# Performance work log

Hardware: AMD Instinct MI355X
Metric: run time of the kernel (lower is better)

## Reference

```python
import jax, jax.numpy as jnp
import numpy as np

B, C, H, W_, N, E = 8, 256, 128, 128, 4096, 128
EPS = 1e-12  # torch F.normalize default eps


def grid_sample_points(x, kpts):
    """Bilinear grid_sample at point coords, padding_mode='zeros', align_corners=False.
    x: [B,C,H,W], kpts: [B,N,2] in [-1,1] (x,y order) -> [B,C,N].
    """
    Bx, Cx, Hx, Wx = x.shape
    # unnormalize (align_corners=False)
    ix = (kpts[..., 0] + 1.0) * (Wx * 0.5) - 0.5  # [B,N]
    iy = (kpts[..., 1] + 1.0) * (Hx * 0.5) - 0.5
    x0f = jnp.floor(ix)
    y0f = jnp.floor(iy)
    wx = ix - x0f  # fractional weights
    wy = iy - y0f
    x0 = x0f.astype(jnp.int32)
    y0 = y0f.astype(jnp.int32)
    x1 = x0 + 1
    y1 = y0 + 1

    def gather(xi, yi):
        valid = (xi >= 0) & (xi < Wx) & (yi >= 0) & (yi < Hx)  # [B,N]
        xc = jnp.clip(xi, 0, Wx - 1)
        yc = jnp.clip(yi, 0, Hx - 1)
        # per-batch gather of [C] vectors at N points -> [B,C,N]
        v = jax.vmap(lambda xb, yy, xx: xb[:, yy, xx])(x, yc, xc)
        return v * valid[:, None, :].astype(x.dtype)

    v00 = gather(x0, y0)
    v10 = gather(x1, y0)
    v01 = gather(x0, y1)
    v11 = gather(x1, y1)
    wxb = wx[:, None, :]
    wyb = wy[:, None, :]
    return (v00 * (1 - wxb) * (1 - wyb)
            + v10 * wxb * (1 - wyb)
            + v01 * (1 - wxb) * wyb
            + v11 * wxb * wyb)


def setup_inputs() -> dict:
    key = jax.random.key(0)
    k1, k2, k3 = jax.random.split(key, 3)
    x = jax.random.normal(k1, (B, C, H, W_), dtype=jnp.float32)
    # keypoints in normalized [-1,1] coords (grid_sample convention)
    kpts = jax.random.uniform(k2, (B, N, 2), dtype=jnp.float32) * 2.0 - 1.0
    # xavier_normal_(gain=0.1) for Linear(C -> E)
    std = 0.1 * np.sqrt(2.0 / (C + E))
    whiten_w = jax.random.normal(k3, (E, C), dtype=jnp.float32) * std
    whiten_b = jnp.zeros((E,), dtype=jnp.float32)
    return {"x": x, "kpts": kpts, "whiten_w": whiten_w, "whiten_b": whiten_b}


def reference(x, kpts, whiten_w, whiten_b):
    desc = grid_sample_points(x, kpts)              # [B,C,N]
    desc = jnp.transpose(desc, (0, 2, 1))           # [B,N,C]
    desc = jnp.einsum('bnc,ec->bne', desc, whiten_w) + whiten_b  # [B,N,E]
    norm = jnp.maximum(jnp.linalg.norm(desc, axis=2, keepdims=True), EPS)
    return desc / norm
```

## Files before the change

kernel.cpp:

```cpp
#include <hip/hip_runtime.h>
#include <hip/hip_bf16.h>
#include <math.h>

#define BB 8
#define CC 256
#define HH 128
#define WW 128
#define NN 4096
#define EE 128

#define WT_OFF   0
#define BASE_OFF 131072
#define WGT_OFF  262144
#define DESC_OFF 786432
#define WS_NEED  (786432ull + (unsigned long long)BB*CC*NN*4ull)

__global__ void coef_kernel(const float* __restrict__ kpts,
                            int* __restrict__ baseb, float4* __restrict__ wgt) {
  int i = blockIdx.x * blockDim.x + threadIdx.x;
  float kx = kpts[2 * i], ky = kpts[2 * i + 1];
  float ix = (kx + 1.f) * (WW * 0.5f) - 0.5f;
  float iy = (ky + 1.f) * (HH * 0.5f) - 0.5f;
  float x0f = floorf(ix), y0f = floorf(iy);
  float wx = ix - x0f, wy = iy - y0f;
  int x0 = (int)x0f, y0 = (int)y0f;
  float ax0 = (x0 >= 0 && x0 < WW) ? (1.f - wx) : 0.f;
  float ax1 = (x0 + 1 >= 0 && x0 + 1 < WW) ? wx : 0.f;
  float ay0 = (y0 >= 0 && y0 < HH) ? (1.f - wy) : 0.f;
  float ay1 = (y0 + 1 >= 0 && y0 + 1 < HH) ? wy : 0.f;
  int bx = min(max(x0, 0), WW - 2);
  int by = min(max(y0, 0), HH - 2);
  float a0 = 0.f, a1 = 0.f, c0 = 0.f, c1 = 0.f;
  if (x0 == bx) a0 += ax0; else if (x0 == bx + 1) a1 += ax0;
  if (x0 + 1 == bx) a0 += ax1; else if (x0 + 1 == bx + 1) a1 += ax1;
  if (y0 == by) c0 += ay0; else if (y0 == by + 1) c1 += ay0;
  if (y0 + 1 == by) c0 += ay1; else if (y0 + 1 == by + 1) c1 += ay1;
  baseb[i] = by * WW + bx;
  wgt[i] = make_float4(a0 * c0, a1 * c0, a0 * c1, a1 * c1);
}

__global__ void wtrans_kernel(const float* __restrict__ W, float* __restrict__ Wt) {
  int i = blockIdx.x * blockDim.x + threadIdx.x;
  int c = i >> 7, e = i & (EE - 1);
  Wt[i] = W[e * CC + c];
}

__global__ __launch_bounds__(256) void gather_kernel(
    const float* __restrict__ x, const int* __restrict__ baseb,
    const float4* __restrict__ wgt, float* __restrict__ desc) {
  __shared__ float plane[HH * WW];
  int blk = blockIdx.x;
  int b = blk >> 8;
  const float4* s4 = (const float4*)(x + ((size_t)blk << 14));
  float4* p4 = (float4*)plane;
  for (int i = threadIdx.x; i < (HH * WW / 4); i += 256) p4[i] = s4[i];
  __syncthreads();
  const int* bb = baseb + b * NN;
  const float4* wb = wgt + b * NN;
  float* dst = desc + ((size_t)blk << 12);
  for (int n = threadIdx.x; n < NN; n += 256) {
    int base = bb[n];
    float4 w = wb[n];
    float v = plane[base] * w.x + plane[base + 1] * w.y
            + plane[base + WW] * w.z + plane[base + WW + 1] * w.w;
    dst[n] = v;
  }
}

__global__ __launch_bounds__(256) void gemm_norm_kernel(
    const float* __restrict__ desc, const float* __restrict__ Wt,
    const float* __restrict__ bias, float* __restrict__ out) {
  __shared__ float4 A4s[32 * 32];
  __shared__ float4 W4s[32 * 32];
  int t = threadIdx.x;
  int blk = blockIdx.x;
  int b = blk >> 5;
  int n0 = (blk & 31) << 7;
  int te = t & 15, tn = t >> 4;
  float acc[8][8];
#pragma unroll
  for (int j = 0; j < 8; ++j)
#pragma unroll
    for (int k = 0; k < 8; ++k) acc[j][k] = 0.f;
  const float4* wt4 = (const float4*)Wt;
  const float4* d4 = (const float4*)desc;
  for (int cb = 0; cb < CC; cb += 32) {
    __syncthreads();
    int base4 = (b * CC + cb) * (NN / 4) + (n0 >> 2);
#pragma unroll
    for (int p = 0; p < 4; ++p) {
      int q = t + 256 * p;
      int cc = q >> 5, ii = q & 31;
      A4s[q] = d4[base4 + cc * (NN / 4) + ii];
      W4s[q] = wt4[(cb + cc) * (EE / 4) + ii];
    }
    __syncthreads();
    for (int cc = 0; cc < 32; ++cc) {
      float4 a0 = A4s[cc * 32 + tn * 2];
      float4 a1 = A4s[cc * 32 + tn * 2 + 1];
      float4 w0 = W4s[cc * 32 + te * 2];
      float4 w1 = W4s[cc * 32 + te * 2 + 1];
      float av[8] = {a0.x, a0.y, a0.z, a0.w, a1.x, a1.y, a1.z, a1.w};
      float wv[8] = {w0.x, w0.y, w0.z, w0.w, w1.x, w1.y, w1.z, w1.w};
#pragma unroll
      for (int j = 0; j < 8; ++j)
#pragma unroll
        for (int k = 0; k < 8; ++k) acc[j][k] += wv[j] * av[k];
    }
  }
  float4 bi0 = *(const float4*)&bias[te * 8];
  float4 bi1 = *(const float4*)&bias[te * 8 + 4];
  float bv[8] = {bi0.x, bi0.y, bi0.z, bi0.w, bi1.x, bi1.y, bi1.z, bi1.w};
#pragma unroll
  for (int j = 0; j < 8; ++j)
#pragma unroll
    for (int k = 0; k < 8; ++k) acc[j][k] += bv[j];
  float4* out4 = (float4*)out;
#pragma unroll
  for (int k = 0; k < 8; ++k) {
    float s = 0.f;
#pragma unroll
    for (int j = 0; j < 8; ++j) s += acc[j][k] * acc[j][k];
    s += __shfl_xor(s, 1); s += __shfl_xor(s, 2);
    s += __shfl_xor(s, 4); s += __shfl_xor(s, 8);
    float inv = 1.f / fmaxf(sqrtf(s), 1e-12f);
    int n = n0 + tn * 8 + k;
    size_t o = ((size_t)(b * NN + n) << 5) + te * 2;
    out4[o]     = make_float4(acc[0][k] * inv, acc[1][k] * inv, acc[2][k] * inv, acc[3][k] * inv);
    out4[o + 1] = make_float4(acc[4][k] * inv, acc[5][k] * inv, acc[6][k] * inv, acc[7][k] * inv);
  }
}

__global__ __launch_bounds__(128) void fused_fallback(
    const float* __restrict__ x, const float* __restrict__ kpts,
    const float* __restrict__ W, const float* __restrict__ bias,
    float* __restrict__ out) {
  __shared__ float dsc[CC];
  __shared__ float sred[2];
  int blk = blockIdx.x;
  int b = blk >> 12;
  float kx = kpts[2 * blk], ky = kpts[2 * blk + 1];
  float ix = (kx + 1.f) * (WW * 0.5f) - 0.5f;
  float iy = (ky + 1.f) * (HH * 0.5f) - 0.5f;
  float x0f = floorf(ix), y0f = floorf(iy);
  float wx = ix - x0f, wy = iy - y0f;
  int x0 = (int)x0f, y0 = (int)y0f;
  float ax0 = (x0 >= 0 && x0 < WW) ? (1.f - wx) : 0.f;
  float ax1 = (x0 + 1 >= 0 && x0 + 1 < WW) ? wx : 0.f;
  float ay0 = (y0 >= 0 && y0 < HH) ? (1.f - wy) : 0.f;
  float ay1 = (y0 + 1 >= 0 && y0 + 1 < HH) ? wy : 0.f;
  int bx = min(max(x0, 0), WW - 2);
  int by = min(max(y0, 0), HH - 2);
  float a0 = 0.f, a1 = 0.f, r0 = 0.f, r1 = 0.f;
  if (x0 == bx) a0 += ax0; else if (x0 == bx + 1) a1 += ax0;
  if (x0 + 1 == bx) a0 += ax1; else if (x0 + 1 == bx + 1) a1 += ax1;
  if (y0 == by) r0 += ay0; else if (y0 == by + 1) r1 += ay0;
  if (y0 + 1 == by) r0 += ay1; else if (y0 + 1 == by + 1) r1 += ay1;
  int base = by * WW + bx;
  float w00 = a0 * r0, w10 = a1 * r0, w01 = a0 * r1, w11 = a1 * r1;
  int t = threadIdx.x;
  const float* src = x + ((size_t)b << 22);
  for (int c = t; c < CC; c += 128) {
    const float* p = src + ((size_t)c << 14);
    dsc[c] = p[base] * w00 + p[base + 1] * w10 + p[base + WW] * w01 + p[base + WW + 1] * w11;
  }
  __syncthreads();
  float acc = bias[t];
  const float* wr = W + t * CC;
  for (int c = 0; c < CC; ++c) acc += wr[c] * dsc[c];
  float s = acc * acc;
  for (int m = 1; m < 64; m <<= 1) s += __shfl_xor(s, m);
  if ((t & 63) == 0) sred[t >> 6] = s;
  __syncthreads();
  float tot = sred[0] + sred[1];
  float inv = 1.f / fmaxf(sqrtf(tot), 1e-12f);
  out[((size_t)blk << 7) + t] = acc * inv;
}

extern "C" void kernel_launch(void* const* d_in, const int* in_sizes, int n_in,
                              void* d_out, int out_size, void* d_ws, size_t ws_size,
                              hipStream_t stream) {
  const float* x    = (const float*)d_in[0];
  const float* kpts = (const float*)d_in[1];
  const float* W    = (const float*)d_in[2];
  const float* bias = (const float*)d_in[3];
  float* out = (float*)d_out;
  if (ws_size >= WS_NEED) {
    char* ws = (char*)d_ws;
    float* Wt    = (float*)(ws + WT_OFF);
    int* baseb   = (int*)(ws + BASE_OFF);
    float4* wgt  = (float4*)(ws + WGT_OFF);
    float* desc  = (float*)(ws + DESC_OFF);
    coef_kernel<<<BB * NN / 128, 128, 0, stream>>>(kpts, baseb, wgt);
    wtrans_kernel<<<CC * EE / 256, 256, 0, stream>>>(W, Wt);
    gather_kernel<<<BB * CC, 256, 0, stream>>>(x, baseb, wgt, desc);
    gemm_norm_kernel<<<BB * (NN / 128), 256, 0, stream>>>(desc, Wt, bias, out);
  } else {
    fused_fallback<<<BB * NN, 128, 0, stream>>>(x, kpts, W, bias, out);
  }
}
```

Baseline: 261.7 us.

## Merge prep kernels, widen gather blocks, shrink GEMM tiles for more blocks

Merges the coefficient and weight-transpose kernels into one prep kernel, which removes a launch. Doubles the gather kernel's block size to 512 threads and fully unrolls its loops. Retiles the GEMM+normalize kernel from 128-point tiles with 8x8 per-thread outputs to 64-point tiles with 4x4 per-thread outputs and 512 threads. This gives 512 blocks instead of 256 and lower register pressure, but less data reuse per thread.

```diff
diff --git a/kernel.cpp b/kernel.cpp
--- a/kernel.cpp
+++ b/kernel.cpp
@@ -15,9 +15,12 @@
 #define DESC_OFF 786432
 #define WS_NEED  (786432ull + (unsigned long long)BB*CC*NN*4ull)
 
-__global__ void coef_kernel(const float* __restrict__ kpts,
-                            int* __restrict__ baseb, float4* __restrict__ wgt) {
+__global__ __launch_bounds__(256) void prep_kernel(
+    const float* __restrict__ kpts, const float* __restrict__ W,
+    int* __restrict__ baseb, float4* __restrict__ wgt, float* __restrict__ Wt) {
   int i = blockIdx.x * blockDim.x + threadIdx.x;
+  int c = i >> 7, e = i & (EE - 1);
+  Wt[i] = W[e * CC + c];
   float kx = kpts[2 * i], ky = kpts[2 * i + 1];
   float ix = (kx + 1.f) * (WW * 0.5f) - 0.5f;
   float iy = (ky + 1.f) * (HH * 0.5f) - 0.5f;
@@ -39,95 +42,93 @@
   wgt[i] = make_float4(a0 * c0, a1 * c0, a0 * c1, a1 * c1);
 }
 
-__global__ void wtrans_kernel(const float* __restrict__ W, float* __restrict__ Wt) {
-  int i = blockIdx.x * blockDim.x + threadIdx.x;
-  int c = i >> 7, e = i & (EE - 1);
-  Wt[i] = W[e * CC + c];
-}
-
-__global__ __launch_bounds__(256) void gather_kernel(
+__global__ __launch_bounds__(512) void gather_kernel(
     const float* __restrict__ x, const int* __restrict__ baseb,
     const float4* __restrict__ wgt, float* __restrict__ desc) {
   __shared__ float plane[HH * WW];
   int blk = blockIdx.x;
   int b = blk >> 8;
+  int t = threadIdx.x;
   const float4* s4 = (const float4*)(x + ((size_t)blk << 14));
   float4* p4 = (float4*)plane;
-  for (int i = threadIdx.x; i < (HH * WW / 4); i += 256) p4[i] = s4[i];
+#pragma unroll
+  for (int i = 0; i < 8; ++i) p4[t + 512 * i] = s4[t + 512 * i];
   __syncthreads();
   const int* bb = baseb + b * NN;
   const float4* wb = wgt + b * NN;
   float* dst = desc + ((size_t)blk << 12);
-  for (int n = threadIdx.x; n < NN; n += 256) {
+#pragma unroll
+  for (int i = 0; i < 8; ++i) {
+    int n = t + 512 * i;
     int base = bb[n];
     float4 w = wb[n];
-    float v = plane[base] * w.x + plane[base + 1] * w.y
-            + plane[base + WW] * w.z + plane[base + WW + 1] * w.w;
-    dst[n] = v;
-  }
-}
-
-__global__ __launch_bounds__(256) void gemm_norm_kernel(
+    dst[n] = plane[base] * w.x + plane[base + 1] * w.y
+           + plane[base + WW] * w.z + plane[base + WW + 1] * w.w;
+  }
+}
+
+__global__ __launch_bounds__(512) void gemm_norm_kernel(
     const float* __restrict__ desc, const float* __restrict__ Wt,
     const float* __restrict__ bias, float* __restrict__ out) {
-  __shared__ float4 A4s[32 * 32];
+  __shared__ float4 A4s[32 * 16];
   __shared__ float4 W4s[32 * 32];
   int t = threadIdx.x;
   int blk = blockIdx.x;
-  int b = blk >> 5;
-  int n0 = (blk & 31) << 7;
-  int te = t & 15, tn = t >> 4;
-  float acc[8][8];
-#pragma unroll
-  for (int j = 0; j < 8; ++j)
-#pragma unroll
-    for (int k = 0; k < 8; ++k) acc[j][k] = 0.f;
+  int b = blk >> 6;
+  int n0 = (blk & 63) << 6;
+  int te = t & 31;
+  int tn = t >> 5;
+  float acc[4][4];
+#pragma unroll
+  for (int j = 0; j < 4; ++j)
+#pragma unroll
+    for (int k = 0; k < 4; ++k) acc[j][k] = 0.f;
   const float4* wt4 = (const float4*)Wt;
   const float4* d4 = (const float4*)desc;
   for (int cb = 0; cb < CC; cb += 32) {
     __syncthreads();
     int base4 = (b * CC + cb) * (NN / 4) + (n0 >> 2);
-#pragma unroll
-    for (int p = 0; p < 4; ++p) {
-      int q = t + 256 * p;
+    {
+      int ccA = t >> 4, iiA = t & 15;
+      A4s[t] = d4[base4 + ccA * (NN / 4) + iiA];
+    }
+#pragma unroll
+    for (int p = 0; p < 2; ++p) {
+      int q = t + 512 * p;
       int cc = q >> 5, ii = q & 31;
-      A4s[q] = d4[base4 + cc * (NN / 4) + ii];
       W4s[q] = wt4[(cb + cc) * (EE / 4) + ii];
     }
     __syncthreads();
+#pragma unroll
     for (int cc = 0; cc < 32; ++cc) {
-      float4 a0 = A4s[cc * 32 + tn * 2];
-      float4 a1 = A4s[cc * 32 + tn * 2 + 1];
-      float4 w0 = W4s[cc * 32 + te * 2];
-      float4 w1 = W4s[cc * 32 + te * 2 + 1];
-      float av[8] = {a0.x, a0.y, a0.z, a0.w, a1.x, a1.y, a1.z, a1.w};
-      float wv[8] = {w0.x, w0.y, w0.z, w0.w, w1.x, w1.y, w1.z, w1.w};
-#pragma unroll
-      for (int j = 0; j < 8; ++j)
-#pragma unroll
-        for (int k = 0; k < 8; ++k) acc[j][k] += wv[j] * av[k];
+      float4 a = A4s[cc * 16 + tn];
+      float4 w = W4s[cc * 32 + te];
+      float av[4] = {a.x, a.y, a.z, a.w};
+      float wv[4] = {w.x, w.y, w.z, w.w};
+#pragma unroll
+      for (int j = 0; j < 4; ++j)
+#pragma unroll
+        for (int k = 0; k < 4; ++k) acc[j][k] += wv[j] * av[k];
     }
   }
-  float4 bi0 = *(const float4*)&bias[te * 8];
-  float4 bi1 = *(const float4*)&bias[te * 8 + 4];
-  float bv[8] = {bi0.x, bi0.y, bi0.z, bi0.w, bi1.x, bi1.y, bi1.z, bi1.w};
-#pragma unroll
-  for (int j = 0; j < 8; ++j)
-#pragma unroll
-    for (int k = 0; k < 8; ++k) acc[j][k] += bv[j];
+  float4 bi = ((const float4*)bias)[te];
+  float bv[4] = {bi.x, bi.y, bi.z, bi.w};
+#pragma unroll
+  for (int j = 0; j < 4; ++j)
+#pragma unroll
+    for (int k = 0; k < 4; ++k) acc[j][k] += bv[j];
   float4* out4 = (float4*)out;
 #pragma unroll
-  for (int k = 0; k < 8; ++k) {
+  for (int k = 0; k < 4; ++k) {
     float s = 0.f;
 #pragma unroll
-    for (int j = 0; j < 8; ++j) s += acc[j][k] * acc[j][k];
-    s += __shfl_xor(s, 1); s += __shfl_xor(s, 2);
-    s += __shfl_xor(s, 4); s += __shfl_xor(s, 8);
+    for (int j = 0; j < 4; ++j) s += acc[j][k] * acc[j][k];
+    s += __shfl_xor(s, 1); s += __shfl_xor(s, 2); s += __shfl_xor(s, 4);
+    s += __shfl_xor(s, 8); s += __shfl_xor(s, 16);
     float inv = 1.f / fmaxf(sqrtf(s), 1e-12f);
-    int n = n0 + tn * 8 + k;
-    size_t o = ((size_t)(b * NN + n) << 5) + te * 2;
-    out4[o]     = make_float4(acc[0][k] * inv, acc[1][k] * inv, acc[2][k] * inv, acc[3][k] * inv);
-    out4[o + 1] = make_float4(acc[4][k] * inv, acc[5][k] * inv, acc[6][k] * inv, acc[7][k] * inv);
+    int n = n0 + tn * 4 + k;
+    out4[((size_t)(b * NN + n) << 5) + te] =
+        make_float4(acc[0][k] * inv, acc[1][k] * inv, acc[2][k] * inv, acc[3][k] * inv);
   }
 }
 
@@ -191,10 +192,9 @@
     int* baseb   = (int*)(ws + BASE_OFF);
     float4* wgt  = (float4*)(ws + WGT_OFF);
     float* desc  = (float*)(ws + DESC_OFF);
-    coef_kernel<<<BB * NN / 128, 128, 0, stream>>>(kpts, baseb, wgt);
-    wtrans_kernel<<<CC * EE / 256, 256, 0, stream>>>(W, Wt);
-    gather_kernel<<<BB * CC, 256, 0, stream>>>(x, baseb, wgt, desc);
-    gemm_norm_kernel<<<BB * (NN / 128), 256, 0, stream>>>(desc, Wt, bias, out);
+    prep_kernel<<<BB * NN / 256, 256, 0, stream>>>(kpts, W, baseb, wgt, Wt);
+    gather_kernel<<<BB * CC, 512, 0, stream>>>(x, baseb, wgt, desc);
+    gemm_norm_kernel<<<BB * (NN / 64), 512, 0, stream>>>(desc, Wt, bias, out);
   } else {
     fused_fallback<<<BB * NN, 128, 0, stream>>>(x, kpts, W, bias, out);
   }
```

Result: faster. 233.1 us (-10.9%).
